# Kernel tuning notes

Measured on AMD Instinct MI355X. Metric: run time of the kernel, lower is better.

Reference implementation:

```python
import jax, jax.numpy as jnp
import numpy as np

B, T, I, H, L = 128, 256, 512, 1024, 2


def setup_inputs() -> dict:
    key = jax.random.key(0)
    ks = jax.random.split(key, 9)
    s_i = 1.0 / np.sqrt(H)
    inp = {
        "x": jax.random.normal(ks[0], (B, T, I), dtype=jnp.float32),
        # layer 0: input_size -> hidden_size
        "W_ih0": jax.random.uniform(ks[1], (4 * H, I), dtype=jnp.float32, minval=-s_i, maxval=s_i),
        "W_hh0": jax.random.uniform(ks[2], (4 * H, H), dtype=jnp.float32, minval=-s_i, maxval=s_i),
        "b_ih0": jax.random.uniform(ks[3], (4 * H,), dtype=jnp.float32, minval=-s_i, maxval=s_i),
        "b_hh0": jax.random.uniform(ks[4], (4 * H,), dtype=jnp.float32, minval=-s_i, maxval=s_i),
        # layer 1: hidden_size -> hidden_size
        "W_ih1": jax.random.uniform(ks[5], (4 * H, H), dtype=jnp.float32, minval=-s_i, maxval=s_i),
        "W_hh1": jax.random.uniform(ks[6], (4 * H, H), dtype=jnp.float32, minval=-s_i, maxval=s_i),
        "b_ih1": jax.random.uniform(ks[7], (4 * H,), dtype=jnp.float32, minval=-s_i, maxval=s_i),
        "b_hh1": jax.random.uniform(ks[8], (4 * H,), dtype=jnp.float32, minval=-s_i, maxval=s_i),
    }
    return inp


def _lstm_cell(xt, h, c, W_ih, W_hh, b_ih, b_hh):
    # gates: [B, 4H] in order i, f, g, o (standard LSTMCell layout)
    gates = xt @ W_ih.T + b_ih + h @ W_hh.T + b_hh
    i, f, g, o = jnp.split(gates, 4, axis=-1)
    c_new = jax.nn.sigmoid(f) * c + jax.nn.sigmoid(i) * jnp.tanh(g)
    h_new = jax.nn.sigmoid(o) * jnp.tanh(c_new)
    return h_new, c_new


def reference(x, W_ih0, W_hh0, b_ih0, b_hh0, W_ih1, W_hh1, b_ih1, b_hh1):
    batch = x.shape[0]
    hidden = W_hh0.shape[1]
    params = ((W_ih0, W_hh0, b_ih0, b_hh0), (W_ih1, W_hh1, b_ih1, b_hh1))
    z = jnp.zeros((batch, hidden), dtype=x.dtype)
    # torch code initializes h and c both from h0 (zeros)
    init = (tuple(z for _ in params), tuple(z for _ in params))

    def step(carry, xt):
        hs, cs = carry
        new_h, new_c = [], []
        layer_in = xt
        for l, (Wi, Wh, bi, bh) in enumerate(params):
            h2, c2 = _lstm_cell(layer_in, hs[l], cs[l], Wi, Wh, bi, bh)
            new_h.append(h2)
            new_c.append(c2)
            layer_in = h2
        return (tuple(new_h), tuple(new_c)), layer_in

    xs = jnp.swapaxes(x, 0, 1)  # [T, B, I]
    _, ys = jax.lax.scan(step, init, xs)
    out = jnp.swapaxes(ys, 0, 1)  # [B, T, H]
    return out
```

## Files before the change

kernel.cpp:

```cpp
#include <hip/hip_runtime.h>

#define B_ 128
#define T_ 256
#define I_ 512
#define H_ 1024

typedef _Float16 f16;
typedef _Float16 v8h __attribute__((ext_vector_type(8)));
typedef _Float16 v2h __attribute__((ext_vector_type(2)));
typedef float v16f __attribute__((ext_vector_type(16)));

__device__ __forceinline__ float fsigmoid(float x) { return 1.0f / (1.0f + __expf(-x)); }
__device__ __forceinline__ float ftanh(float x) { return 1.0f - 2.0f / (__expf(2.0f * x) + 1.0f); }

__device__ __forceinline__ void gl_lds16(const void* g, void* l) {
    __builtin_amdgcn_global_load_lds(
        (const __attribute__((address_space(1))) unsigned int*)g,
        (__attribute__((address_space(3))) unsigned int*)l, 16, 0, 0);
}
__device__ __forceinline__ void gl_lds16_coh(const void* g, void* l) {
    __builtin_amdgcn_global_load_lds(
        (const __attribute__((address_space(1))) unsigned int*)g,
        (__attribute__((address_space(3))) unsigned int*)l, 16, 0, 17);
}
__device__ __forceinline__ void poll4(const int* p0, const int* p1, const int* p2, const int* p3,
                                      int& a, int& b, int& c, int& d) {
    asm volatile("global_load_dword %0, %4, off sc0 sc1\n\t"
                 "global_load_dword %1, %5, off sc0 sc1\n\t"
                 "global_load_dword %2, %6, off sc0 sc1\n\t"
                 "global_load_dword %3, %7, off sc0 sc1\n\t"
                 "s_waitcnt vmcnt(0)"
                 : "=&v"(a), "=&v"(b), "=&v"(c), "=&v"(d)
                 : "v"(p0), "v"(p1), "v"(p2), "v"(p3)
                 : "memory");
}

__global__ void k_f32_to_f16(const float* __restrict__ in, f16* __restrict__ out, int n) {
    int i = blockIdx.x * blockDim.x + threadIdx.x;
    int st = gridDim.x * blockDim.x;
    for (; i < n; i += st) out[i] = (f16)in[i];
}
__global__ void k_bias_sum(const float* __restrict__ a, const float* __restrict__ b,
                           float* __restrict__ o, int n) {
    int i = blockIdx.x * blockDim.x + threadIdx.x;
    int st = gridDim.x * blockDim.x;
    for (; i < n; i += st) o[i] = a[i] + b[i];
}

template <int SLOT>
__device__ void run_slot4(int mh, int tile, int widx128,
                          const f16* __restrict__ xh,
                          const f16* __restrict__ wi, const f16* __restrict__ wh,
                          const float* __restrict__ bs,
                          f16* __restrict__ h0, f16* __restrict__ h1,
                          float* __restrict__ out, int* flags, char* lds)
{
    constexpr int K0 = SLOT ? 1024 : 512;
    constexpr int KW = SLOT ? 512 : 384;
    constexpr int NR = KW / 64;
    constexpr int NKS = KW / 16;
    const size_t BH = (size_t)B_ * H_;

    const int tid = threadIdx.x;
    const int wave = tid >> 6;
    const int lane = tid & 63;
    const int l31 = lane & 31, khi = lane >> 5;
    const int nw = wave & 1, kw = wave >> 1;
    const int n0 = tile * 16;
    const int rbase = mh * 64;

    const int gcl = nw * 32 + l31;
    const size_t gr = (size_t)(gcl >> 4) * H_ + n0 + (gcl & 15);
    v8h wfrag[NKS];
#pragma unroll
    for (int s = 0; s < NKS; ++s) {
        const int k = kw * KW + s * 16 + khi * 8;
        const f16* p = (k < K0) ? (wi + gr * K0 + k) : (wh + gr * H_ + (k - K0));
        wfrag[s] = *(const v8h*)p;
    }

    const int urow = tid >> 3;
    const int un = (tid & 7) * 2;
    const float2 bI = *(const float2*)(bs + 0 * H_ + n0 + un);
    const float2 bF = *(const float2*)(bs + 1 * H_ + n0 + un);
    const float2 bG = *(const float2*)(bs + 2 * H_ + n0 + un);
    const float2 bO = *(const float2*)(bs + 3 * H_ + n0 + un);
    float c0r = 0.f, c1r = 0.f;

    int* f_own = flags + SLOT * 512;
    int* f_oth = flags + (1 - SLOT) * 512;

    float* red = (float*)lds;
    float* r2b = (float*)(lds + 32768);
    float* gf  = (float*)(lds + 49152);

    const int rw_ = lane >> 3;
    const int ss_ = (lane & 7) ^ rw_;

#pragma unroll 1
    for (int p = 0; p <= T_; ++p) {
        const bool active = SLOT ? (p >= 1) : (p < T_);
        const int tau = SLOT ? p - 1 : p;

        const f16* srcA = nullptr; size_t strA = 0; const f16* srcB = nullptr; f16* hout = nullptr;
        if (active) {
            if (SLOT == 0) {
                srcA = xh + (size_t)tau * I_;  strA = (size_t)T_ * I_;
                srcB = h0 + (size_t)((p + 3) & 3) * BH;
                hout = h0 + (size_t)(p & 3) * BH;
            } else {
                srcA = h0 + (size_t)((p + 3) & 3) * BH;  strA = H_;
                srcB = h1 + (size_t)((p + 1) & 1) * BH;
                hout = h1 + (size_t)(p & 1) * BH;
            }
        }

        auto issue = [&](int r) {
            const int kc = kw * KW + r * 64;
            const f16* base; size_t str; int koff; bool coh;
            if (kc < K0) { base = srcA; str = strA; koff = kc; coh = (SLOT == 1); }
            else         { base = srcB; str = (size_t)H_; koff = kc - K0; coh = true; }
            char* dbase = lds + kw * 32768 + (r & 3) * 8192 + nw * 4096;
#pragma unroll
            for (int i = 0; i < 4; ++i) {
                const int rl = rbase + nw * 32 + i * 8 + rw_;
                const f16* gp = base + (size_t)rl * str + koff + ss_ * 8;
                if (coh) gl_lds16_coh(gp, dbase + i * 1024);
                else     gl_lds16(gp, dbase + i * 1024);
            }
        };

        unsigned premask = 0;
        if (active && SLOT == 0) {
#pragma unroll
            for (int r = 0; r < 3; ++r)
                if (kw * KW + r * 64 + 64 <= K0) { issue(r); premask |= 1u << r; }
        }

        {
            const int t_own = p;
            const int t_oth = SLOT ? p : (p >= 2 ? p - 2 : 0);
            if (wave == 0) {
                const int* o0 = f_own + lane * 4;
                const int* o1 = f_own + (lane + 64) * 4;
                const int* q0 = f_oth + lane * 4;
                const int* q1 = f_oth + (lane + 64) * 4;
                for (;;) {
                    int a, b, c, d;
                    poll4(o0, o1, q0, q1, a, b, c, d);
                    if (__ballot(a >= t_own && b >= t_own && c >= t_oth && d >= t_oth) == ~0ULL) break;
                    __builtin_amdgcn_s_sleep(1);
                }
            }
            __syncthreads();
            __builtin_amdgcn_sched_barrier(0);
        }

        if (active) {
#pragma unroll
            for (int r = 0; r < 3; ++r)
                if (!(premask & (1u << r))) issue(r);

            v16f acc0 = {}, acc1 = {};

#pragma unroll
            for (int r = 0; r < NR; ++r) {
                if (r < NR - 2)       asm volatile("s_waitcnt vmcnt(8)" ::: "memory");
                else if (r == NR - 2) asm volatile("s_waitcnt vmcnt(4)" ::: "memory");
                else                  asm volatile("s_waitcnt vmcnt(0)" ::: "memory");
                __builtin_amdgcn_s_barrier();
                __builtin_amdgcn_sched_barrier(0);
                if (r + 3 < NR) issue(r + 3);
                const char* sb = lds + kw * 32768 + (r & 3) * 8192;
#pragma unroll
                for (int ks = 0; ks < 4; ++ks) {
                    const int qo = (((ks * 2 + khi) ^ (l31 & 7)) << 4);
                    const v8h a0 = *(const v8h*)(sb + l31 * 128 + qo);
                    const v8h a1 = *(const v8h*)(sb + (32 + l31) * 128 + qo);
                    __builtin_amdgcn_s_setprio(1);
                    acc0 = __builtin_amdgcn_mfma_f32_32x32x16_f16(a0, wfrag[r * 4 + ks], acc0, 0, 0, 0);
                    acc1 = __builtin_amdgcn_mfma_f32_32x32x16_f16(a1, wfrag[r * 4 + ks], acc1, 0, 0, 0);
                    __builtin_amdgcn_s_setprio(0);
                }
            }
            __syncthreads();

            if (kw >= 2) {
                float* rg = red + ((kw - 2) * 2 + nw) * 2048;
#pragma unroll
                for (int j = 0; j < 16; ++j) {
                    rg[j * 64 + lane] = acc0[j];
                    rg[(16 + j) * 64 + lane] = acc1[j];
                }
            }
            __syncthreads();
            if (kw < 2) {
                const float* rg = red + (kw * 2 + nw) * 2048;
#pragma unroll
                for (int j = 0; j < 16; ++j) {
                    acc0[j] += rg[j * 64 + lane];
                    acc1[j] += rg[(16 + j) * 64 + lane];
                }
                if (kw == 1) {
                    float* rr = r2b + nw * 2048;
#pragma unroll
                    for (int j = 0; j < 16; ++j) {
                        rr[j * 64 + lane] = acc0[j];
                        rr[(16 + j) * 64 + lane] = acc1[j];
                    }
                }
            }
            __syncthreads();
            if (kw == 0) {
                const float* rr = r2b + nw * 2048;
#pragma unroll
                for (int j = 0; j < 16; ++j) {
                    const int row = (j & 3) + 8 * (j >> 2) + 4 * khi;
                    gf[row * 68 + nw * 32 + l31] = acc0[j] + rr[j * 64 + lane];
                    gf[(32 + row) * 68 + nw * 32 + l31] = acc1[j] + rr[(16 + j) * 64 + lane];
                }
            }
            __syncthreads();

            {
                const float* g0 = gf + urow * 68 + un;
                const float xi0 = g0[0] + bI.x,  xi1 = g0[1] + bI.y;
                const float xf0 = g0[16] + bF.x, xf1 = g0[17] + bF.y;
                const float xg0 = g0[32] + bG.x, xg1 = g0[33] + bG.y;
                const float xo0 = g0[48] + bO.x, xo1 = g0[49] + bO.y;
                const float cn0 = fsigmoid(xf0) * c0r + fsigmoid(xi0) * ftanh(xg0);
                const float cn1 = fsigmoid(xf1) * c1r + fsigmoid(xi1) * ftanh(xg1);
                const float hn0 = fsigmoid(xo0) * ftanh(cn0);
                const float hn1 = fsigmoid(xo1) * ftanh(cn1);
                c0r = cn0; c1r = cn1;
                union { v2h h2; unsigned u; } cv;
                cv.h2[0] = (f16)hn0; cv.h2[1] = (f16)hn1;
                unsigned* hp = (unsigned*)(hout + (size_t)(rbase + urow) * H_ + n0 + un);
                asm volatile("global_store_dword %0, %1, off sc0 sc1" :: "v"(hp), "v"(cv.u) : "memory");
                if (SLOT == 1) {
                    float2 yv; yv.x = hn0; yv.y = hn1;
                    *(float2*)(out + ((size_t)(rbase + urow) * T_ + tau) * H_ + n0 + un) = yv;
                }
            }
        }

        asm volatile("s_waitcnt vmcnt(0)" ::: "memory");
        __syncthreads();
        if (tid == 0) {
            int v = p + 1;
            int* fp = f_own + widx128 * 4;
            asm volatile("global_store_dword %0, %1, off sc0 sc1" :: "v"(fp), "v"(v) : "memory");
        }
    }
}

__global__ __launch_bounds__(512, 2) void lstm_persist4(
    const f16* __restrict__ xh,
    const f16* __restrict__ w0i, const f16* __restrict__ w0h,
    const f16* __restrict__ w1i, const f16* __restrict__ w1h,
    const float* __restrict__ bs0, const float* __restrict__ bs1,
    f16* __restrict__ h0, f16* __restrict__ h1, float* __restrict__ out,
    int* flags)
{
    __shared__ __align__(16) char lds[131072];
    const int bx = blockIdx.x;
    const int slot = bx & 1;
    const int mh = (bx >> 1) & 1;
    const int tile = bx >> 2;
    const int widx128 = mh * 64 + tile;
    if (slot == 0)
        run_slot4<0>(mh, tile, widx128, xh, w0i, w0h, bs0, h0, h1, out, flags, lds);
    else
        run_slot4<1>(mh, tile, widx128, xh, w1i, w1h, bs1, h0, h1, out, flags, lds);
}

#define BM 64
#define NT 8

__global__ __launch_bounds__(256) void lstm_step(
    const float* __restrict__ A1, long a1_stride, int K1,
    const float* __restrict__ hprev,
    const float* __restrict__ Wih, const float* __restrict__ Whh,
    const float* __restrict__ bih, const float* __restrict__ bhh,
    float* __restrict__ cbuf, float* __restrict__ hout,
    float* yout, long y_stride)
{
    __shared__ float As[32][66];
    __shared__ float Ws[32][36];
    const int tid = threadIdx.x;
    const int n0 = blockIdx.x * NT;
    const int b0 = blockIdx.y * BM;
    const int tb = tid >> 3;
    const int tc = tid & 7;
    const int lr = tid >> 3;
    const int lk = tid & 7;
    const long wj = (long)(lr >> 3) * H_ + n0 + (lr & 7);
    float acc[2][4] = {{0.f, 0.f, 0.f, 0.f}, {0.f, 0.f, 0.f, 0.f}};
#pragma unroll 1
    for (int ph = 0; ph < 2; ++ph) {
        const float* Ap = (ph == 0) ? A1 : hprev;
        const long as = (ph == 0) ? a1_stride : (long)H_;
        const float* W = (ph == 0) ? Wih : Whh;
        const int K = (ph == 0) ? K1 : H_;
        const float* arow0 = Ap + (long)(b0 + lr) * as + 4 * lk;
        const float* arow1 = Ap + (long)(b0 + lr + 32) * as + 4 * lk;
        const float* wrow = W + wj * K + 4 * lk;
        float4 ra0 = *(const float4*)(arow0);
        float4 ra1 = *(const float4*)(arow1);
        float4 rw = *(const float4*)(wrow);
        for (int k0 = 0; k0 < K; k0 += 32) {
            __syncthreads();
            {
                const int kk = 4 * lk;
                As[kk + 0][lr] = ra0.x; As[kk + 1][lr] = ra0.y;
                As[kk + 2][lr] = ra0.z; As[kk + 3][lr] = ra0.w;
                As[kk + 0][lr + 32] = ra1.x; As[kk + 1][lr + 32] = ra1.y;
                As[kk + 2][lr + 32] = ra1.z; As[kk + 3][lr + 32] = ra1.w;
                Ws[kk + 0][lr] = rw.x; Ws[kk + 1][lr] = rw.y;
                Ws[kk + 2][lr] = rw.z; Ws[kk + 3][lr] = rw.w;
            }
            __syncthreads();
            const int kn = k0 + 32;
            if (kn < K) {
                ra0 = *(const float4*)(arow0 + kn);
                ra1 = *(const float4*)(arow1 + kn);
                rw = *(const float4*)(wrow + kn);
            }
#pragma unroll
            for (int k = 0; k < 32; ++k) {
                float2 a = *(const float2*)&As[k][2 * tb];
                float4 w = *(const float4*)&Ws[k][4 * tc];
                acc[0][0] = fmaf(a.x, w.x, acc[0][0]);
                acc[0][1] = fmaf(a.x, w.y, acc[0][1]);
                acc[0][2] = fmaf(a.x, w.z, acc[0][2]);
                acc[0][3] = fmaf(a.x, w.w, acc[0][3]);
                acc[1][0] = fmaf(a.y, w.x, acc[1][0]);
                acc[1][1] = fmaf(a.y, w.y, acc[1][1]);
                acc[1][2] = fmaf(a.y, w.z, acc[1][2]);
                acc[1][3] = fmaf(a.y, w.w, acc[1][3]);
            }
        }
    }
    __syncthreads();
    float* gsf = &As[0][0];
#pragma unroll
    for (int bi = 0; bi < 2; ++bi)
#pragma unroll
        for (int ci = 0; ci < 4; ++ci)
            gsf[(2 * tb + bi) * 33 + 4 * tc + ci] = acc[bi][ci];
    __syncthreads();
    const int dn = tid & 7;
    const int bq = tid >> 3;
    const int n = n0 + dn;
#pragma unroll
    for (int s = 0; s < 2; ++s) {
        const int b = bq + 32 * s;
        float xi = gsf[b * 33 + dn] + bih[n] + bhh[n];
        float xf = gsf[b * 33 + 8 + dn] + bih[H_ + n] + bhh[H_ + n];
        float xg = gsf[b * 33 + 16 + dn] + bih[2 * H_ + n] + bhh[2 * H_ + n];
        float xo = gsf[b * 33 + 24 + dn] + bih[3 * H_ + n] + bhh[3 * H_ + n];
        const long idx = (long)(b0 + b) * H_ + n;
        const float c_old = cbuf[idx];
        const float cn = fsigmoid(xf) * c_old + fsigmoid(xi) * ftanh(xg);
        const float hn = fsigmoid(xo) * ftanh(cn);
        cbuf[idx] = cn;
        hout[idx] = hn;
        if (yout) yout[(long)(b0 + b) * y_stride + n] = hn;
    }
}

extern "C" void kernel_launch(void* const* d_in, const int* in_sizes, int n_in,
                              void* d_out, int out_size, void* d_ws, size_t ws_size,
                              hipStream_t stream) {
    const float* x = (const float*)d_in[0];
    const float* Wih0 = (const float*)d_in[1];
    const float* Whh0 = (const float*)d_in[2];
    const float* bih0 = (const float*)d_in[3];
    const float* bhh0 = (const float*)d_in[4];
    const float* Wih1 = (const float*)d_in[5];
    const float* Whh1 = (const float*)d_in[6];
    const float* bih1 = (const float*)d_in[7];
    const float* bhh1 = (const float*)d_in[8];
    float* out = (float*)d_out;

    const size_t BH = (size_t)B_ * H_;
    const size_t NX = (size_t)B_ * T_ * I_;
    const size_t NW0I = (size_t)4 * H_ * I_;
    const size_t NWH = (size_t)4 * H_ * H_;

    const size_t off_xh = 0;
    const size_t off_w0i = off_xh + NX * 2;
    const size_t off_w0h = off_w0i + NW0I * 2;
    const size_t off_w1i = off_w0h + NWH * 2;
    const size_t off_w1h = off_w1i + NWH * 2;
    const size_t off_bs0 = off_w1h + NWH * 2;
    const size_t off_bs1 = off_bs0 + 4 * H_ * 4;
    const size_t off_h0 = off_bs1 + 4 * H_ * 4;
    const size_t off_h1 = off_h0 + 4 * BH * 2;
    const size_t off_flags = off_h1 + 2 * BH * 2;
    const size_t REQ = off_flags + 1024 * 4;

    char* ws = (char*)d_ws;

    if (ws_size >= REQ) {
        f16* xh = (f16*)(ws + off_xh);
        f16* w0i = (f16*)(ws + off_w0i);
        f16* w0h = (f16*)(ws + off_w0h);
        f16* w1i = (f16*)(ws + off_w1i);
        f16* w1h = (f16*)(ws + off_w1h);
        float* bs0 = (float*)(ws + off_bs0);
        float* bs1 = (float*)(ws + off_bs1);
        f16* h0 = (f16*)(ws + off_h0);
        f16* h1 = (f16*)(ws + off_h1);
        int* flags = (int*)(ws + off_flags);

        hipMemsetAsync(ws + off_h0, 0, REQ - off_h0, stream);

        dim3 cb(256);
        k_f32_to_f16<<<2048, cb, 0, stream>>>(x, xh, (int)NX);
        k_f32_to_f16<<<2048, cb, 0, stream>>>(Wih0, w0i, (int)NW0I);
        k_f32_to_f16<<<2048, cb, 0, stream>>>(Whh0, w0h, (int)NWH);
        k_f32_to_f16<<<2048, cb, 0, stream>>>(Wih1, w1i, (int)NWH);
        k_f32_to_f16<<<2048, cb, 0, stream>>>(Whh1, w1h, (int)NWH);
        k_bias_sum<<<16, cb, 0, stream>>>(bih0, bhh0, bs0, 4 * H_);
        k_bias_sum<<<16, cb, 0, stream>>>(bih1, bhh1, bs1, 4 * H_);

        lstm_persist4<<<256, 512, 0, stream>>>(xh, w0i, w0h, w1i, w1h, bs0, bs1,
                                               h0, h1, out, flags);
        return;
    }

    float* fws = (float*)d_ws;
    float* h0a = fws;
    float* h0b = fws + BH;
    float* c0 = fws + 2 * BH;
    float* h1a = fws + 3 * BH;
    float* h1b = fws + 4 * BH;
    float* c1 = fws + 5 * BH;
    hipMemsetAsync(d_ws, 0, 6 * BH * sizeof(float), stream);

    dim3 grid(H_ / NT, B_ / BM);
    dim3 block(256);
    for (int t = 0; t < T_; ++t) {
        float* h0in = (t & 1) ? h0b : h0a;
        float* h0out = (t & 1) ? h0a : h0b;
        float* h1in = (t & 1) ? h1b : h1a;
        float* h1out = (t & 1) ? h1a : h1b;
        lstm_step<<<grid, block, 0, stream>>>(
            x + (size_t)t * I_, (long)T_ * I_, I_,
            h0in, Wih0, Whh0, bih0, bhh0, c0, h0out, nullptr, 0);
        lstm_step<<<grid, block, 0, stream>>>(
            h0out, (long)H_, H_,
            h1in, Wih1, Whh1, bih1, bhh1, c1, h1out,
            out + (size_t)t * H_, (long)T_ * H_);
    }
}
```

Before: 2.403 ms.

## Replace block-wide flag polling and barriers with per-wave split waits and pairwise LDS counters

Inter-block step synchronisation is restructured so that separate waves poll the own-layer and other-layer flags, with flags packed one int per block and read as dwordx4. Waits are published through LDS condition words, so waves that need only the input half can start before the recurrent half's dependencies are ready. The per-chunk s_barrier is replaced by a pairwise LDS counter handshake between the two k-waves sharing a buffer, and the next prefetch is issued after the MFMAs rather than before them. Layer-1 h is quadruple-buffered to relax the reuse hazard. The changes aim to cut synchronisation latency on the recurrent critical path, but the spin-waits add risk of ordering bugs or hangs.

```diff
diff --git a/kernel.cpp b/kernel.cpp
--- a/kernel.cpp
+++ b/kernel.cpp
@@ -9,6 +9,7 @@
 typedef _Float16 v8h __attribute__((ext_vector_type(8)));
 typedef _Float16 v2h __attribute__((ext_vector_type(2)));
 typedef float v16f __attribute__((ext_vector_type(16)));
+typedef int v4i __attribute__((ext_vector_type(4)));
 
 __device__ __forceinline__ float fsigmoid(float x) { return 1.0f / (1.0f + __expf(-x)); }
 __device__ __forceinline__ float ftanh(float x) { return 1.0f - 2.0f / (__expf(2.0f * x) + 1.0f); }
@@ -23,16 +24,20 @@
         (const __attribute__((address_space(1))) unsigned int*)g,
         (__attribute__((address_space(3))) unsigned int*)l, 16, 0, 17);
 }
-__device__ __forceinline__ void poll4(const int* p0, const int* p1, const int* p2, const int* p3,
-                                      int& a, int& b, int& c, int& d) {
-    asm volatile("global_load_dword %0, %4, off sc0 sc1\n\t"
-                 "global_load_dword %1, %5, off sc0 sc1\n\t"
-                 "global_load_dword %2, %6, off sc0 sc1\n\t"
-                 "global_load_dword %3, %7, off sc0 sc1\n\t"
-                 "s_waitcnt vmcnt(0)"
-                 : "=&v"(a), "=&v"(b), "=&v"(c), "=&v"(d)
-                 : "v"(p0), "v"(p1), "v"(p2), "v"(p3)
-                 : "memory");
+
+__device__ __forceinline__ void pollwait(const int* base, int tgt, int lane) {
+    if (tgt <= 0) return;
+    for (;;) {
+        bool ok = true;
+        if (lane < 32) {
+            v4i v;
+            asm volatile("global_load_dwordx4 %0, %1, off sc0 sc1\n\ts_waitcnt vmcnt(0)"
+                         : "=&v"(v) : "v"(base + lane * 4) : "memory");
+            ok = (v[0] >= tgt) && (v[1] >= tgt) && (v[2] >= tgt) && (v[3] >= tgt);
+        }
+        if (__ballot(ok) == ~0ULL) return;
+        __builtin_amdgcn_s_sleep(1);
+    }
 }
 
 __global__ void k_f32_to_f16(const float* __restrict__ in, f16* __restrict__ out, int n) {
@@ -48,7 +53,7 @@
 }
 
 template <int SLOT>
-__device__ void run_slot4(int mh, int tile, int widx128,
+__device__ void run_slot5(int mh, int tile, int widx128,
                           const f16* __restrict__ xh,
                           const f16* __restrict__ wi, const f16* __restrict__ wh,
                           const float* __restrict__ bs,
@@ -87,8 +92,12 @@
     const float2 bO = *(const float2*)(bs + 3 * H_ + n0 + un);
     float c0r = 0.f, c1r = 0.f;
 
-    int* f_own = flags + SLOT * 512;
-    int* f_oth = flags + (1 - SLOT) * 512;
+    int* f_own = flags + SLOT * 128;
+    int* f_oth = flags + (1 - SLOT) * 128;
+
+    volatile int* condA = (volatile int*)(lds + 131072);
+    volatile int* condB = (volatile int*)(lds + 131076);
+    volatile int* ctrs  = (volatile int*)(lds + 131080);
 
     float* red = (float*)lds;
     float* r2b = (float*)(lds + 32768);
@@ -96,6 +105,10 @@
 
     const int rw_ = lane >> 3;
     const int ss_ = (lane & 7) ^ rw_;
+
+    if (tid == 0) { *condA = -1; *condB = -1; }
+    if (tid < 8) ctrs[tid] = 0;
+    __syncthreads();
 
 #pragma unroll 1
     for (int p = 0; p <= T_; ++p) {
@@ -110,8 +123,8 @@
                 hout = h0 + (size_t)(p & 3) * BH;
             } else {
                 srcA = h0 + (size_t)((p + 3) & 3) * BH;  strA = H_;
-                srcB = h1 + (size_t)((p + 1) & 1) * BH;
-                hout = h1 + (size_t)(p & 1) * BH;
+                srcB = h1 + (size_t)((p + 3) & 3) * BH;
+                hout = h1 + (size_t)(p & 3) * BH;
             }
         }
 
@@ -130,33 +143,42 @@
             }
         };
 
-        unsigned premask = 0;
-        if (active && SLOT == 0) {
-#pragma unroll
-            for (int r = 0; r < 3; ++r)
-                if (kw * KW + r * 64 + 64 <= K0) { issue(r); premask |= 1u << r; }
-        }
-
-        {
-            const int t_own = p;
-            const int t_oth = SLOT ? p : (p >= 2 ? p - 2 : 0);
-            if (wave == 0) {
-                const int* o0 = f_own + lane * 4;
-                const int* o1 = f_own + (lane + 64) * 4;
-                const int* q0 = f_oth + lane * 4;
-                const int* q1 = f_oth + (lane + 64) * 4;
-                for (;;) {
-                    int a, b, c, d;
-                    poll4(o0, o1, q0, q1, a, b, c, d);
-                    if (__ballot(a >= t_own && b >= t_own && c >= t_oth && d >= t_oth) == ~0ULL) break;
-                    __builtin_amdgcn_s_sleep(1);
-                }
-            }
-            __syncthreads();
+        if (active) {
+            unsigned premask = 0;
+            if (SLOT == 0) {
+#pragma unroll
+                for (int r = 0; r < 3; ++r)
+                    if (kw * KW + r * 64 + 64 <= K0) { issue(r); premask |= 1u << r; }
+            }
+
+            if (SLOT == 0) {
+                if (wave == 0) {
+                    pollwait(f_oth, p - 2, lane);
+                    if (lane == 0) { asm volatile("" ::: "memory"); *condB = p; }
+                } else if (wave == 2) {
+                    pollwait(f_own, p, lane);
+                    if (lane == 0) { asm volatile("" ::: "memory"); *condA = p; }
+                } else if (wave >= 3) {
+                    while (*condA < p) __builtin_amdgcn_s_sleep(1);
+                    asm volatile("" ::: "memory");
+                }
+            } else {
+                if (wave == 0) {
+                    pollwait(f_oth, p, lane);
+                    if (lane == 0) { asm volatile("" ::: "memory"); *condA = p; }
+                } else if (wave <= 3) {
+                    while (*condA < p) __builtin_amdgcn_s_sleep(1);
+                    asm volatile("" ::: "memory");
+                } else if (wave == 4) {
+                    pollwait(f_own, p, lane);
+                    if (lane == 0) { asm volatile("" ::: "memory"); *condB = p; }
+                } else {
+                    while (*condB < p) __builtin_amdgcn_s_sleep(1);
+                    asm volatile("" ::: "memory");
+                }
+            }
             __builtin_amdgcn_sched_barrier(0);
-        }
-
-        if (active) {
+
 #pragma unroll
             for (int r = 0; r < 3; ++r)
                 if (!(premask & (1u << r))) issue(r);
@@ -165,12 +187,18 @@
 
 #pragma unroll
             for (int r = 0; r < NR; ++r) {
-                if (r < NR - 2)       asm volatile("s_waitcnt vmcnt(8)" ::: "memory");
-                else if (r == NR - 2) asm volatile("s_waitcnt vmcnt(4)" ::: "memory");
-                else                  asm volatile("s_waitcnt vmcnt(0)" ::: "memory");
-                __builtin_amdgcn_s_barrier();
+                if (r + 2 < NR)      asm volatile("s_waitcnt vmcnt(8)" ::: "memory");
+                else if (r + 1 < NR) asm volatile("s_waitcnt vmcnt(4)" ::: "memory");
+                else                 asm volatile("s_waitcnt vmcnt(0)" ::: "memory");
+                asm volatile("s_waitcnt lgkmcnt(0)" ::: "memory");
+                const int hv = p * 16 + r + 1;
+                if (lane == 0) ctrs[wave] = hv;
+                {
+                    volatile int* pc = ctrs + (wave ^ 1);
+                    while (*pc < hv) { }
+                }
+                asm volatile("" ::: "memory");
                 __builtin_amdgcn_sched_barrier(0);
-                if (r + 3 < NR) issue(r + 3);
                 const char* sb = lds + kw * 32768 + (r & 3) * 8192;
 #pragma unroll
                 for (int ks = 0; ks < 4; ++ks) {
@@ -182,6 +210,7 @@
                     acc1 = __builtin_amdgcn_mfma_f32_32x32x16_f16(a1, wfrag[r * 4 + ks], acc1, 0, 0, 0);
                     __builtin_amdgcn_s_setprio(0);
                 }
+                if (r + 3 < NR) issue(r + 3);
             }
             __syncthreads();
 
@@ -248,13 +277,13 @@
         __syncthreads();
         if (tid == 0) {
             int v = p + 1;
-            int* fp = f_own + widx128 * 4;
+            int* fp = f_own + widx128;
             asm volatile("global_store_dword %0, %1, off sc0 sc1" :: "v"(fp), "v"(v) : "memory");
         }
     }
 }
 
-__global__ __launch_bounds__(512, 2) void lstm_persist4(
+__global__ __launch_bounds__(512, 2) void lstm_persist7(
     const f16* __restrict__ xh,
     const f16* __restrict__ w0i, const f16* __restrict__ w0h,
     const f16* __restrict__ w1i, const f16* __restrict__ w1h,
@@ -262,16 +291,16 @@
     f16* __restrict__ h0, f16* __restrict__ h1, float* __restrict__ out,
     int* flags)
 {
-    __shared__ __align__(16) char lds[131072];
+    __shared__ __align__(16) char lds[131200];
     const int bx = blockIdx.x;
     const int slot = bx & 1;
     const int mh = (bx >> 1) & 1;
     const int tile = bx >> 2;
     const int widx128 = mh * 64 + tile;
     if (slot == 0)
-        run_slot4<0>(mh, tile, widx128, xh, w0i, w0h, bs0, h0, h1, out, flags, lds);
+        run_slot5<0>(mh, tile, widx128, xh, w0i, w0h, bs0, h0, h1, out, flags, lds);
     else
-        run_slot4<1>(mh, tile, widx128, xh, w1i, w1h, bs1, h0, h1, out, flags, lds);
+        run_slot5<1>(mh, tile, widx128, xh, w1i, w1h, bs1, h0, h1, out, flags, lds);
 }
 
 #define BM 64
@@ -397,8 +426,8 @@
     const size_t off_bs1 = off_bs0 + 4 * H_ * 4;
     const size_t off_h0 = off_bs1 + 4 * H_ * 4;
     const size_t off_h1 = off_h0 + 4 * BH * 2;
-    const size_t off_flags = off_h1 + 2 * BH * 2;
-    const size_t REQ = off_flags + 1024 * 4;
+    const size_t off_flags = off_h1 + 4 * BH * 2;
+    const size_t REQ = off_flags + 256 * 4;
 
     char* ws = (char*)d_ws;
 
@@ -425,7 +454,7 @@
         k_bias_sum<<<16, cb, 0, stream>>>(bih0, bhh0, bs0, 4 * H_);
         k_bias_sum<<<16, cb, 0, stream>>>(bih1, bhh1, bs1, 4 * H_);
 
-        lstm_persist4<<<256, 512, 0, stream>>>(xh, w0i, w0h, w1i, w1h, bs0, bs1,
+        lstm_persist7<<<256, 512, 0, stream>>>(xh, w0i, w0h, w1i, w1h, bs0, bs1,
                                                h0, h1, out, flags);
         return;
     }
```

Measured after the change: 2.815 ms. 17.1% more time.
